# Kernel tuning notes

Hardware: AMD Instinct MI355X
Metric: run time of the kernel (lower is better)

Reference implementation:

```python
import jax, jax.numpy as jnp
import numpy as np

B, T, O, D, H = 8, 256, 16, 512, 8
HD = D // H
EPS = 1e-5


def setup_inputs() -> dict:
    key = jax.random.key(0)
    ks = jax.random.split(key, 12)
    s = 1.0 / np.sqrt(D)
    inp = {
        "organ_states": jax.random.normal(ks[0], (B, T, O, D), dtype=jnp.float32),
        "organ_mask": jax.random.randint(ks[1], (B, T, O), 0, 2) > 0,
        "Wq": jax.random.uniform(ks[2], (D, D), jnp.float32, -s, s),
        "bq": jnp.zeros((D,), jnp.float32),
        "Wk": jax.random.uniform(ks[3], (D, D), jnp.float32, -s, s),
        "bk": jnp.zeros((D,), jnp.float32),
        "Wv": jax.random.uniform(ks[4], (D, D), jnp.float32, -s, s),
        "bv": jnp.zeros((D,), jnp.float32),
        "Wo": jax.random.uniform(ks[5], (D, D), jnp.float32, -s, s),
        "bo": jnp.zeros((D,), jnp.float32),
        "gamma": jnp.ones((D,), jnp.float32),
        "beta": jnp.zeros((D,), jnp.float32),
    }
    return inp


def reference(organ_states, organ_mask, Wq, bq, Wk, bk, Wv, bv, Wo, bo, gamma, beta):
    x = organ_states  # (B, T, O, D)
    b, t, o, d = x.shape

    def heads(y):  # (B,T,O,D) -> (B,O,H,T,HD)
        return y.reshape(b, t, o, H, HD).transpose(0, 2, 3, 1, 4)

    q = heads(jnp.einsum('btod,de->btoe', x, Wq) + bq)
    k = heads(jnp.einsum('btod,de->btoe', x, Wk) + bk)
    v = heads(jnp.einsum('btod,de->btoe', x, Wv) + bv)

    scores = jnp.einsum('bohqd,bohkd->bohqk', q, k) / np.sqrt(HD).astype(np.float32)
    # key mask: (B,T,O) -> (B,O,1,1,T)
    mk = organ_mask.transpose(0, 2, 1)[:, :, None, None, :]
    scores = jnp.where(mk, scores, -jnp.inf)
    attn = jax.nn.softmax(scores, axis=-1)
    attn = jnp.where(mk, attn, 0.0)

    att = jnp.einsum('bohqk,bohkd->bohqd', attn, v)  # (B,O,H,T,HD)
    att = att.transpose(0, 3, 1, 2, 4).reshape(b, t, o, d)  # (B,T,O,D)

    out = jnp.einsum('btod,de->btoe', att, Wo) + bo
    res = out + x
    mu = jnp.mean(res, axis=-1, keepdims=True)
    var = jnp.mean(jnp.square(res - mu), axis=-1, keepdims=True)
    y = (res - mu) / jnp.sqrt(var + EPS) * gamma + beta
    y = y * organ_mask[..., None].astype(y.dtype)
    return y
```

## Files before the change

### kernel.cpp

```cpp
#include <hip/hip_runtime.h>


typedef __attribute__((ext_vector_type(8))) short bf16x8;
typedef __attribute__((ext_vector_type(4))) float f32x4;

#define MFMA16(a, b, c) __builtin_amdgcn_mfma_f32_16x16x32_bf16((a), (b), (c), 0, 0, 0)

__device__ __forceinline__ unsigned short f2bf(float f) {
  unsigned int u = __builtin_bit_cast(unsigned int, f);
  u += 0x7fffu + ((u >> 16) & 1u);
  return (unsigned short)(u >> 16);
}

__device__ __forceinline__ void gload_lds16(const void* g, void* lds) {
  __builtin_amdgcn_global_load_lds((__attribute__((address_space(1))) void*)g,
                                   (__attribute__((address_space(3))) void*)lds,
                                   16, 0, 0);
}

#define WS_XB   0ull
#define WS_WT   33554432ull
#define WS_Q    35651584ull
#define WS_K    69206016ull
#define WS_V    102760448ull
#define WS_MASK 136314880ull

__global__ void k_cvt_x(const float* __restrict__ x, unsigned short* __restrict__ xb) {
  int i = blockIdx.x * 256 + threadIdx.x;
  float4 v = ((const float4*)x)[i];
  ushort4 o;
  o.x = f2bf(v.x); o.y = f2bf(v.y); o.z = f2bf(v.z); o.w = f2bf(v.w);
  ((ushort4*)xb)[i] = o;
}

__global__ void k_prep_w(const float* __restrict__ Wq, const float* __restrict__ Wk,
                         const float* __restrict__ Wv, const float* __restrict__ Wo,
                         unsigned short* __restrict__ Wt) {
  int ep = blockIdx.x;
  const float* src; int e;
  if (ep < 512)       { src = Wq; e = ep; }
  else if (ep < 1024) { src = Wk; e = ep - 512; }
  else if (ep < 1536) { src = Wv; e = ep - 1024; }
  else                { src = Wo; e = ep - 1536; }
  for (int d = threadIdx.x; d < 512; d += 256)
    Wt[(size_t)ep * 512 + d] = f2bf(src[(size_t)d * 512 + e]);
}

__global__ void k_prep_mask(const void* __restrict__ mraw, unsigned char* __restrict__ mout) {
  const unsigned int* u = (const unsigned int*)mraw;
  int lane = threadIdx.x & 63;
  int packed = __any(u[lane] > 1u);
  int idx = blockIdx.x * 256 + threadIdx.x;
  unsigned char m;
  if (packed) m = ((const unsigned char*)mraw)[idx] ? 1 : 0;
  else        m = u[idx] ? 1 : 0;
  mout[idx] = m;
}

__global__ __launch_bounds__(512) void k_qkv(
    const unsigned short* __restrict__ Xb, const unsigned short* __restrict__ Wt,
    const float* __restrict__ bq, const float* __restrict__ bk, const float* __restrict__ bv,
    unsigned short* __restrict__ Qb, unsigned short* __restrict__ Kb, unsigned short* __restrict__ Vb) {
  __shared__ char sm[73728];
  const int tid = threadIdx.x, l = tid & 63, w = tid >> 6;
  const int lane15 = l & 15, quad = l >> 4;
  const int rbase = blockIdx.x * 64, which = blockIdx.y;
  const char* xg = (const char*)Xb;
  const char* wgp = (const char*)(Wt + (size_t)which * 512 * 512);
  const int srow = tid >> 3;
  const int c16 = (tid & 7) * 16;
  const int swz_a = c16 ^ ((srow & 7) << 4);
  char* adst = sm + w * 1024;
  f32x4 acc[4][4] = {};
  for (int ks = 0; ks < 8; ++ks) {
    __syncthreads();
    gload_lds16(xg + (size_t)(rbase + srow) * 1024 + ks * 128 + swz_a, adst);
#pragma unroll
    for (int p = 0; p < 8; ++p) {
      int er = p * 64 + srow;
      gload_lds16(wgp + (size_t)er * 1024 + ks * 128 + (c16 ^ ((er & 7) << 4)),
                  sm + 8192 + p * 8192 + w * 1024);
    }
    __syncthreads();
#pragma unroll
    for (int kc = 0; kc < 2; ++kc) {
      bf16x8 af[4], bfr[4];
#pragma unroll
      for (int mt = 0; mt < 4; ++mt) {
        int row = mt * 16 + lane15;
        int byt = (row * 128 + kc * 64 + quad * 16) ^ ((row & 7) << 4);
        af[mt] = *(const bf16x8*)(sm + byt);
      }
#pragma unroll
      for (int nt = 0; nt < 4; ++nt) {
        int col = w * 64 + nt * 16 + lane15;
        int byt = (col * 128 + kc * 64 + quad * 16) ^ ((col & 7) << 4);
        bfr[nt] = *(const bf16x8*)(sm + 8192 + byt);
      }
#pragma unroll
      for (int mt = 0; mt < 4; ++mt)
#pragma unroll
        for (int nt = 0; nt < 4; ++nt)
          acc[mt][nt] = MFMA16(af[mt], bfr[nt], acc[mt][nt]);
    }
  }
  const float* bias = (which == 0) ? bq : (which == 1) ? bk : bv;
  unsigned short* dst = (which == 0) ? Qb : (which == 1) ? Kb : Vb;
#pragma unroll
  for (int mt = 0; mt < 4; ++mt) {
#pragma unroll
    for (int reg = 0; reg < 4; ++reg) {
      int r = rbase + mt * 16 + quad * 4 + reg;
      int b = r >> 12, t = (r >> 4) & 255, o = r & 15;
      size_t base_bt = (size_t)((b * 16 + o) * 8 + w) * 16384 + (size_t)t * 64;
#pragma unroll
      for (int nt = 0; nt < 4; ++nt) {
        int e = w * 64 + nt * 16 + lane15;
        float v = acc[mt][nt][reg] + bias[e];
        dst[base_bt + nt * 16 + lane15] = f2bf(v);
      }
    }
  }
}

__global__ __launch_bounds__(512) void k_attn(
    const unsigned short* __restrict__ Qb, const unsigned short* __restrict__ Kb,
    const unsigned short* __restrict__ Vb, const unsigned char* __restrict__ Mc,
    unsigned short* __restrict__ att) {
  __shared__ char sm[50176];
  const int tid = threadIdx.x, l = tid & 63, w = tid >> 6;
  const int lane15 = l & 15, quad = l >> 4;
  const int bid = blockIdx.x;
  const int h = bid & 7, o = (bid >> 3) & 15, b = bid >> 7;
  const size_t head = (size_t)((b * 16 + o) * 8 + h) * 16384;
  const char* kg = (const char*)(Kb + head);
  const char* vg = (const char*)(Vb + head);
  const unsigned short* qh = Qb + head;
  float* maskb = (float*)(sm + 49152);
  if (tid < 256)
    maskb[tid] = Mc[(size_t)(b * 256 + tid) * 16 + o] ? 0.0f : -30000.0f;
  const int q0 = w * 32;
  bf16x8 qf[2][2];
#pragma unroll
  for (int mt = 0; mt < 2; ++mt)
#pragma unroll
    for (int kc = 0; kc < 2; ++kc)
      qf[mt][kc] = *(const bf16x8*)(qh + (size_t)(q0 + mt * 16 + lane15) * 64 + kc * 32 + quad * 8);
  f32x4 pv[2][4] = {};
  float mrun[2][4], srun[2][4];
#pragma unroll
  for (int mt = 0; mt < 2; ++mt)
#pragma unroll
    for (int reg = 0; reg < 4; ++reg) { mrun[mt][reg] = -30000.0f; srun[mt][reg] = 0.0f; }
  const int srow = tid >> 3;
  const int c16 = (tid & 7) * 16;
  char* kdst = sm + w * 1024;
  char* pbase = sm + 16384 + w * 4096;
  for (int c = 0; c < 4; ++c) {
    __syncthreads();
    gload_lds16(kg + (size_t)(c * 64 + srow) * 128 + (c16 ^ ((srow & 7) << 4)), kdst);
    {
      int tl = tid >> 3, hd0 = (tid & 7) * 8;
      bf16x8 vv = *(const bf16x8*)(vg + (size_t)(c * 64 + tl) * 128 + hd0 * 2);
#pragma unroll
      for (int j = 0; j < 8; ++j) {
        int hd = hd0 + j;
        int byt = (hd * 128 + tl * 2) ^ ((hd & 7) << 4);
        *(unsigned short*)(sm + 8192 + byt) = (unsigned short)vv[j];
      }
    }
    __syncthreads();
    f32x4 sacc[2][4] = {};
#pragma unroll
    for (int kc = 0; kc < 2; ++kc) {
      bf16x8 kf[4];
#pragma unroll
      for (int nt = 0; nt < 4; ++nt) {
        int key = nt * 16 + lane15;
        int byt = (key * 128 + kc * 64 + quad * 16) ^ ((key & 7) << 4);
        kf[nt] = *(const bf16x8*)(sm + byt);
      }
#pragma unroll
      for (int mt = 0; mt < 2; ++mt)
#pragma unroll
        for (int nt = 0; nt < 4; ++nt)
          sacc[mt][nt] = MFMA16(qf[mt][kc], kf[nt], sacc[mt][nt]);
    }
    float bias_v[4];
#pragma unroll
    for (int nt = 0; nt < 4; ++nt) bias_v[nt] = maskb[c * 64 + nt * 16 + lane15];
#pragma unroll
    for (int mt = 0; mt < 2; ++mt) {
#pragma unroll
      for (int nt = 0; nt < 4; ++nt)
#pragma unroll
        for (int reg = 0; reg < 4; ++reg)
          sacc[mt][nt][reg] = sacc[mt][nt][reg] * 0.125f + bias_v[nt];
#pragma unroll
      for (int reg = 0; reg < 4; ++reg) {
        float mx = fmaxf(fmaxf(sacc[mt][0][reg], sacc[mt][1][reg]),
                         fmaxf(sacc[mt][2][reg], sacc[mt][3][reg]));
#pragma unroll
        for (int d = 1; d < 16; d <<= 1) mx = fmaxf(mx, __shfl_xor(mx, d));
        float mnew = fmaxf(mrun[mt][reg], mx);
        float fac = __expf(mrun[mt][reg] - mnew);
        mrun[mt][reg] = mnew;
        float rs = 0.f;
#pragma unroll
        for (int nt = 0; nt < 4; ++nt) {
          float p = __expf(sacc[mt][nt][reg] - mnew);
          sacc[mt][nt][reg] = p;
          rs += p;
        }
#pragma unroll
        for (int d = 1; d < 16; d <<= 1) rs += __shfl_xor(rs, d);
        srun[mt][reg] = srun[mt][reg] * fac + rs;
#pragma unroll
        for (int nh = 0; nh < 4; ++nh) pv[mt][nh][reg] *= fac;
      }
    }
#pragma unroll
    for (int mt = 0; mt < 2; ++mt)
#pragma unroll
      for (int nt = 0; nt < 4; ++nt)
#pragma unroll
        for (int reg = 0; reg < 4; ++reg) {
          int qrow = mt * 16 + quad * 4 + reg;
          int byt = (qrow * 128 + (nt * 16 + lane15) * 2) ^ ((qrow & 7) << 4);
          *(unsigned short*)(pbase + byt) = f2bf(sacc[mt][nt][reg]);
        }
#pragma unroll
    for (int kc = 0; kc < 2; ++kc) {
      bf16x8 pa[2], vbr[4];
#pragma unroll
      for (int mt = 0; mt < 2; ++mt) {
        int qrow = mt * 16 + lane15;
        int byt = (qrow * 128 + kc * 64 + quad * 16) ^ ((qrow & 7) << 4);
        pa[mt] = *(const bf16x8*)(pbase + byt);
      }
#pragma unroll
      for (int nh = 0; nh < 4; ++nh) {
        int hdr = nh * 16 + lane15;
        int byt = (hdr * 128 + kc * 64 + quad * 16) ^ ((hdr & 7) << 4);
        vbr[nh] = *(const bf16x8*)(sm + 8192 + byt);
      }
#pragma unroll
      for (int mt = 0; mt < 2; ++mt)
#pragma unroll
        for (int nh = 0; nh < 4; ++nh)
          pv[mt][nh] = MFMA16(pa[mt], vbr[nh], pv[mt][nh]);
    }
  }
#pragma unroll
  for (int mt = 0; mt < 2; ++mt) {
#pragma unroll
    for (int reg = 0; reg < 4; ++reg) {
      int q = q0 + mt * 16 + quad * 4 + reg;
      float inv = srun[mt][reg] > 0.f ? 1.0f / srun[mt][reg] : 0.f;
      size_t r = (size_t)(b * 256 + q) * 16 + o;
#pragma unroll
      for (int nh = 0; nh < 4; ++nh) {
        int e = h * 64 + nh * 16 + lane15;
        att[r * 512 + e] = f2bf(pv[mt][nh][reg] * inv);
      }
    }
  }
}

__global__ __launch_bounds__(512) void k_oproj(
    const unsigned short* __restrict__ A, const unsigned short* __restrict__ Wt,
    const float* __restrict__ bo, const float* __restrict__ X,
    const unsigned char* __restrict__ Mc, const float* __restrict__ gamma,
    const float* __restrict__ beta, float* __restrict__ out) {
  __shared__ char sm[73728];
  __shared__ float psum[64][8];
  __shared__ float psumsq[64][8];
  __shared__ float smean[64];
  __shared__ float srstd[64];
  const int tid = threadIdx.x, l = tid & 63, w = tid >> 6;
  const int lane15 = l & 15, quad = l >> 4;
  const int rbase = blockIdx.x * 64;
  const char* ag = (const char*)A;
  const char* wgp = (const char*)(Wt + (size_t)1536 * 512);
  const int srow = tid >> 3;
  const int c16 = (tid & 7) * 16;
  const int swz_a = c16 ^ ((srow & 7) << 4);
  char* adst = sm + w * 1024;
  f32x4 acc[4][4] = {};
  for (int ks = 0; ks < 8; ++ks) {
    __syncthreads();
    gload_lds16(ag + (size_t)(rbase + srow) * 1024 + ks * 128 + swz_a, adst);
#pragma unroll
    for (int p = 0; p < 8; ++p) {
      int er = p * 64 + srow;
      gload_lds16(wgp + (size_t)er * 1024 + ks * 128 + (c16 ^ ((er & 7) << 4)),
                  sm + 8192 + p * 8192 + w * 1024);
    }
    __syncthreads();
#pragma unroll
    for (int kc = 0; kc < 2; ++kc) {
      bf16x8 af[4], bfr[4];
#pragma unroll
      for (int mt = 0; mt < 4; ++mt) {
        int row = mt * 16 + lane15;
        int byt = (row * 128 + kc * 64 + quad * 16) ^ ((row & 7) << 4);
        af[mt] = *(const bf16x8*)(sm + byt);
      }
#pragma unroll
      for (int nt = 0; nt < 4; ++nt) {
        int col = w * 64 + nt * 16 + lane15;
        int byt = (col * 128 + kc * 64 + quad * 16) ^ ((col & 7) << 4);
        bfr[nt] = *(const bf16x8*)(sm + 8192 + byt);
      }
#pragma unroll
      for (int mt = 0; mt < 4; ++mt)
#pragma unroll
        for (int nt = 0; nt < 4; ++nt)
          acc[mt][nt] = MFMA16(af[mt], bfr[nt], acc[mt][nt]);
    }
  }
#pragma unroll
  for (int mt = 0; mt < 4; ++mt) {
#pragma unroll
    for (int reg = 0; reg < 4; ++reg) {
      int rl = mt * 16 + quad * 4 + reg;
      int r = rbase + rl;
      float s1 = 0.f, s2 = 0.f;
#pragma unroll
      for (int nt = 0; nt < 4; ++nt) {
        int col = w * 64 + nt * 16 + lane15;
        float v = acc[mt][nt][reg] + bo[col] + X[(size_t)r * 512 + col];
        acc[mt][nt][reg] = v;
        s1 += v; s2 += v * v;
      }
#pragma unroll
      for (int d = 1; d < 16; d <<= 1) { s1 += __shfl_xor(s1, d); s2 += __shfl_xor(s2, d); }
      if (lane15 == 0) { psum[rl][w] = s1; psumsq[rl][w] = s2; }
    }
  }
  __syncthreads();
  if (tid < 64) {
    float a = 0.f, q = 0.f;
#pragma unroll
    for (int j = 0; j < 8; ++j) { a += psum[tid][j]; q += psumsq[tid][j]; }
    float mu = a * (1.f / 512.f);
    float var = q * (1.f / 512.f) - mu * mu;
    smean[tid] = mu;
    srstd[tid] = rsqrtf(fmaxf(var, 0.f) + 1e-5f);
  }
  __syncthreads();
#pragma unroll
  for (int mt = 0; mt < 4; ++mt) {
#pragma unroll
    for (int reg = 0; reg < 4; ++reg) {
      int rl = mt * 16 + quad * 4 + reg;
      int r = rbase + rl;
      float mu = smean[rl], rs = srstd[rl];
      float mkf = Mc[r] ? 1.f : 0.f;
#pragma unroll
      for (int nt = 0; nt < 4; ++nt) {
        int col = w * 64 + nt * 16 + lane15;
        float y = (acc[mt][nt][reg] - mu) * rs * gamma[col] + beta[col];
        out[(size_t)r * 512 + col] = y * mkf;
      }
    }
  }
}

extern "C" void kernel_launch(void* const* d_in, const int* in_sizes, int n_in,
                              void* d_out, int out_size, void* d_ws, size_t ws_size,
                              hipStream_t stream) {
  const float* X     = (const float*)d_in[0];
  const void*  Mraw  = d_in[1];
  const float* Wq    = (const float*)d_in[2];
  const float* bq    = (const float*)d_in[3];
  const float* Wk    = (const float*)d_in[4];
  const float* bk    = (const float*)d_in[5];
  const float* Wv    = (const float*)d_in[6];
  const float* bv    = (const float*)d_in[7];
  const float* Wo    = (const float*)d_in[8];
  const float* bo    = (const float*)d_in[9];
  const float* gamma = (const float*)d_in[10];
  const float* beta  = (const float*)d_in[11];

  char* ws = (char*)d_ws;
  unsigned short* Xb  = (unsigned short*)(ws + WS_XB);
  unsigned short* Wt  = (unsigned short*)(ws + WS_WT);
  unsigned short* Qb  = (unsigned short*)(ws + WS_Q);
  unsigned short* Kb  = (unsigned short*)(ws + WS_K);
  unsigned short* Vb  = (unsigned short*)(ws + WS_V);
  unsigned char*  Mc  = (unsigned char*)(ws + WS_MASK);
  unsigned short* att = Xb;

  hipLaunchKernelGGL(k_cvt_x,    dim3(16384),   dim3(256), 0, stream, X, Xb);
  hipLaunchKernelGGL(k_prep_w,   dim3(2048),    dim3(256), 0, stream, Wq, Wk, Wv, Wo, Wt);
  hipLaunchKernelGGL(k_prep_mask,dim3(128),     dim3(256), 0, stream, Mraw, Mc);
  hipLaunchKernelGGL(k_qkv,      dim3(512, 3),  dim3(512), 0, stream, Xb, Wt, bq, bk, bv, Qb, Kb, Vb);
  hipLaunchKernelGGL(k_attn,     dim3(1024),    dim3(512), 0, stream, Qb, Kb, Vb, Mc, att);
  hipLaunchKernelGGL(k_oproj,    dim3(512),     dim3(512), 0, stream, att, Wt, bo, X, Mc, gamma, beta,
                     (float*)d_out);
}
```

Baseline: 305.0 us.

## Load full K/V head into LDS once and use single-pass softmax in attention

```diff
diff --git a/kernel.cpp b/kernel.cpp
--- a/kernel.cpp
+++ b/kernel.cpp
@@ -123,22 +123,30 @@
   }
 }
 
-__global__ __launch_bounds__(512) void k_attn(
+__global__ __launch_bounds__(512, 2) void k_attn(
     const unsigned short* __restrict__ Qb, const unsigned short* __restrict__ Kb,
     const unsigned short* __restrict__ Vb, const unsigned char* __restrict__ Mc,
     unsigned short* __restrict__ att) {
-  __shared__ char sm[50176];
+  __shared__ char sm[99328];
   const int tid = threadIdx.x, l = tid & 63, w = tid >> 6;
   const int lane15 = l & 15, quad = l >> 4;
   const int bid = blockIdx.x;
   const int h = bid & 7, o = (bid >> 3) & 15, b = bid >> 7;
   const size_t head = (size_t)((b * 16 + o) * 8 + h) * 16384;
+  const unsigned short* qh = Qb + head;
   const char* kg = (const char*)(Kb + head);
-  const char* vg = (const char*)(Vb + head);
-  const unsigned short* qh = Qb + head;
-  float* maskb = (float*)(sm + 49152);
-  if (tid < 256)
-    maskb[tid] = Mc[(size_t)(b * 256 + tid) * 16 + o] ? 0.0f : -30000.0f;
+  const unsigned short* vh = Vb + head;
+
+  {
+    const int srow = tid >> 3;
+    const int c16 = (tid & 7) * 16;
+    char* kdst = sm + w * 1024;
+#pragma unroll
+    for (int i = 0; i < 4; ++i) {
+      int t = i * 64 + srow;
+      gload_lds16(kg + (size_t)t * 128 + (c16 ^ ((t & 7) << 4)), kdst + i * 8192);
+    }
+  }
   const int q0 = w * 32;
   bf16x8 qf[2][2];
 #pragma unroll
@@ -146,79 +154,87 @@
 #pragma unroll
     for (int kc = 0; kc < 2; ++kc)
       qf[mt][kc] = *(const bf16x8*)(qh + (size_t)(q0 + mt * 16 + lane15) * 64 + kc * 32 + quad * 8);
-  f32x4 pv[2][4] = {};
-  float mrun[2][4], srun[2][4];
-#pragma unroll
-  for (int mt = 0; mt < 2; ++mt)
-#pragma unroll
-    for (int reg = 0; reg < 4; ++reg) { mrun[mt][reg] = -30000.0f; srun[mt][reg] = 0.0f; }
-  const int srow = tid >> 3;
-  const int c16 = (tid & 7) * 16;
-  char* kdst = sm + w * 1024;
-  char* pbase = sm + 16384 + w * 4096;
+  unsigned short vreg[32];
+  {
+    const int hd = tid & 63, tq = tid >> 6;
+#pragma unroll
+    for (int i = 0; i < 4; ++i)
+#pragma unroll
+      for (int j = 0; j < 8; ++j)
+        vreg[i * 8 + j] = vh[(size_t)(tq * 32 + i * 8 + j) * 64 + hd];
+  }
+  float* maskb = (float*)(sm + 98304);
+  if (tid < 256)
+    maskb[tid] = Mc[(size_t)(b * 256 + tid) * 16 + o] ? 0.0f : -43280.0f;
+  {
+    const int hd = tid & 63, tq = tid >> 6;
+    const int rowb = 32768 + hd * 512;
+    const int swz = (hd & 7) << 4;
+#pragma unroll
+    for (int i = 0; i < 4; ++i) {
+      bf16x8 pk;
+#pragma unroll
+      for (int j = 0; j < 8; ++j) pk[j] = (short)vreg[i * 8 + j];
+      int t0 = tq * 32 + i * 8;
+      *(bf16x8*)(sm + rowb + ((t0 * 2) ^ swz)) = pk;
+    }
+  }
+  __syncthreads();
+
+  f32x4 sacc[2][16] = {};
+#pragma unroll
   for (int c = 0; c < 4; ++c) {
-    __syncthreads();
-    gload_lds16(kg + (size_t)(c * 64 + srow) * 128 + (c16 ^ ((srow & 7) << 4)), kdst);
-    {
-      int tl = tid >> 3, hd0 = (tid & 7) * 8;
-      bf16x8 vv = *(const bf16x8*)(vg + (size_t)(c * 64 + tl) * 128 + hd0 * 2);
-#pragma unroll
-      for (int j = 0; j < 8; ++j) {
-        int hd = hd0 + j;
-        int byt = (hd * 128 + tl * 2) ^ ((hd & 7) << 4);
-        *(unsigned short*)(sm + 8192 + byt) = (unsigned short)vv[j];
-      }
-    }
-    __syncthreads();
-    f32x4 sacc[2][4] = {};
 #pragma unroll
     for (int kc = 0; kc < 2; ++kc) {
       bf16x8 kf[4];
 #pragma unroll
       for (int nt = 0; nt < 4; ++nt) {
-        int key = nt * 16 + lane15;
-        int byt = (key * 128 + kc * 64 + quad * 16) ^ ((key & 7) << 4);
+        int t = c * 64 + nt * 16 + lane15;
+        int byt = t * 128 + ((kc * 64 + quad * 16) ^ ((t & 7) << 4));
         kf[nt] = *(const bf16x8*)(sm + byt);
       }
 #pragma unroll
       for (int mt = 0; mt < 2; ++mt)
 #pragma unroll
         for (int nt = 0; nt < 4; ++nt)
-          sacc[mt][nt] = MFMA16(qf[mt][kc], kf[nt], sacc[mt][nt]);
-    }
-    float bias_v[4];
-#pragma unroll
-    for (int nt = 0; nt < 4; ++nt) bias_v[nt] = maskb[c * 64 + nt * 16 + lane15];
-#pragma unroll
-    for (int mt = 0; mt < 2; ++mt) {
-#pragma unroll
-      for (int nt = 0; nt < 4; ++nt)
-#pragma unroll
-        for (int reg = 0; reg < 4; ++reg)
-          sacc[mt][nt][reg] = sacc[mt][nt][reg] * 0.125f + bias_v[nt];
-#pragma unroll
-      for (int reg = 0; reg < 4; ++reg) {
-        float mx = fmaxf(fmaxf(sacc[mt][0][reg], sacc[mt][1][reg]),
-                         fmaxf(sacc[mt][2][reg], sacc[mt][3][reg]));
-#pragma unroll
-        for (int d = 1; d < 16; d <<= 1) mx = fmaxf(mx, __shfl_xor(mx, d));
-        float mnew = fmaxf(mrun[mt][reg], mx);
-        float fac = __expf(mrun[mt][reg] - mnew);
-        mrun[mt][reg] = mnew;
-        float rs = 0.f;
-#pragma unroll
-        for (int nt = 0; nt < 4; ++nt) {
-          float p = __expf(sacc[mt][nt][reg] - mnew);
-          sacc[mt][nt][reg] = p;
-          rs += p;
-        }
-#pragma unroll
-        for (int d = 1; d < 16; d <<= 1) rs += __shfl_xor(rs, d);
-        srun[mt][reg] = srun[mt][reg] * fac + rs;
-#pragma unroll
-        for (int nh = 0; nh < 4; ++nh) pv[mt][nh][reg] *= fac;
-      }
-    }
+          sacc[mt][c * 4 + nt] = MFMA16(qf[mt][kc], kf[nt], sacc[mt][c * 4 + nt]);
+    }
+  }
+
+  float biasv[16];
+#pragma unroll
+  for (int g = 0; g < 16; ++g) biasv[g] = maskb[g * 16 + lane15];
+  float inv[2][4];
+#pragma unroll
+  for (int mt = 0; mt < 2; ++mt) {
+#pragma unroll
+    for (int reg = 0; reg < 4; ++reg) {
+      float v[16];
+#pragma unroll
+      for (int g = 0; g < 16; ++g)
+        v[g] = sacc[mt][g][reg] * 0.18033688f + biasv[g];
+      float m = v[0];
+#pragma unroll
+      for (int g = 1; g < 16; ++g) m = fmaxf(m, v[g]);
+#pragma unroll
+      for (int d = 1; d < 16; d <<= 1) m = fmaxf(m, __shfl_xor(m, d));
+      float rs = 0.f;
+#pragma unroll
+      for (int g = 0; g < 16; ++g) {
+        float p = __builtin_amdgcn_exp2f(v[g] - m);
+        sacc[mt][g][reg] = p;
+        rs += p;
+      }
+#pragma unroll
+      for (int d = 1; d < 16; d <<= 1) rs += __shfl_xor(rs, d);
+      inv[mt][reg] = 1.0f / rs;
+    }
+  }
+
+  char* pb = sm + 65536 + w * 4096;
+  f32x4 pv[2][4] = {};
+#pragma unroll
+  for (int c = 0; c < 4; ++c) {
 #pragma unroll
     for (int mt = 0; mt < 2; ++mt)
 #pragma unroll
@@ -227,7 +243,7 @@
         for (int reg = 0; reg < 4; ++reg) {
           int qrow = mt * 16 + quad * 4 + reg;
           int byt = (qrow * 128 + (nt * 16 + lane15) * 2) ^ ((qrow & 7) << 4);
-          *(unsigned short*)(pbase + byt) = f2bf(sacc[mt][nt][reg]);
+          *(unsigned short*)(pb + byt) = f2bf(sacc[mt][c * 4 + nt][reg]);
         }
 #pragma unroll
     for (int kc = 0; kc < 2; ++kc) {
@@ -236,13 +252,13 @@
       for (int mt = 0; mt < 2; ++mt) {
         int qrow = mt * 16 + lane15;
         int byt = (qrow * 128 + kc * 64 + quad * 16) ^ ((qrow & 7) << 4);
-        pa[mt] = *(const bf16x8*)(pbase + byt);
+        pa[mt] = *(const bf16x8*)(pb + byt);
       }
 #pragma unroll
       for (int nh = 0; nh < 4; ++nh) {
-        int hdr = nh * 16 + lane15;
-        int byt = (hdr * 128 + kc * 64 + quad * 16) ^ ((hdr & 7) << 4);
-        vbr[nh] = *(const bf16x8*)(sm + 8192 + byt);
+        int hd = nh * 16 + lane15;
+        int byt = hd * 512 + ((c * 128 + kc * 64 + quad * 16) ^ ((hd & 7) << 4));
+        vbr[nh] = *(const bf16x8*)(sm + 32768 + byt);
       }
 #pragma unroll
       for (int mt = 0; mt < 2; ++mt)
@@ -251,18 +267,17 @@
           pv[mt][nh] = MFMA16(pa[mt], vbr[nh], pv[mt][nh]);
     }
   }
+
 #pragma unroll
   for (int mt = 0; mt < 2; ++mt) {
 #pragma unroll
     for (int reg = 0; reg < 4; ++reg) {
       int q = q0 + mt * 16 + quad * 4 + reg;
-      float inv = srun[mt][reg] > 0.f ? 1.0f / srun[mt][reg] : 0.f;
       size_t r = (size_t)(b * 256 + q) * 16 + o;
-#pragma unroll
-      for (int nh = 0; nh < 4; ++nh) {
-        int e = h * 64 + nh * 16 + lane15;
-        att[r * 512 + e] = f2bf(pv[mt][nh][reg] * inv);
-      }
+      float iv = inv[mt][reg];
+#pragma unroll
+      for (int nh = 0; nh < 4; ++nh)
+        att[r * 512 + h * 64 + nh * 16 + lane15] = f2bf(pv[mt][nh][reg] * iv);
     }
   }
 }
```

Result: faster. 295.1 us (-3.2%).
